# Performance work log

Hardware: AMD Instinct MI355X
Metric: run time of the kernel (lower is better)

The kernel has to match this reference:

```python
import jax, jax.numpy as jnp
import numpy as np

N_NODES = 50000


def gcn_conv(x, W, b, src, dst):
    # PyG GCNConv: h = x @ W; add self-loops; norm = deg^{-1/2}[src]*deg^{-1/2}[dst];
    # out = scatter_add(norm * h[src] -> dst) + bias
    h = x @ W  # [N, out]
    ones = jnp.ones(src.shape[0], dtype=x.dtype)
    deg = jax.ops.segment_sum(ones, dst, num_segments=N_NODES) + 1.0  # +1 for self-loop
    inv_sqrt = deg ** -0.5
    norm = inv_sqrt[src] * inv_sqrt[dst]  # [E]
    msgs = h[src] * norm[:, None]  # [E, out]
    agg = jax.ops.segment_sum(msgs, dst, num_segments=N_NODES)
    # self-loop contribution: norm_ii = deg_i^{-1}
    agg = agg + h * (inv_sqrt * inv_sqrt)[:, None]
    return agg + b


def setup_inputs() -> dict:
    key = jax.random.key(0)
    k1, k2, k3, k4 = jax.random.split(key, 4)
    d_in, d_h = 256, 256
    x = jax.random.normal(k1, (N_NODES, d_in), dtype=jnp.float32)
    edge_index = jax.random.randint(k2, (2, 800000), 0, N_NODES, dtype=jnp.int64)
    # Glorot-style params (GCNConv linear has no bias; separate bias added post-agg)
    W1 = jax.random.normal(k3, (d_in, d_h), dtype=jnp.float32) / np.sqrt(d_in)
    W2 = jax.random.normal(k4, (d_h, d_h), dtype=jnp.float32) / np.sqrt(d_h)
    b1 = jnp.zeros((d_h,), dtype=jnp.float32)
    b2 = jnp.zeros((d_h,), dtype=jnp.float32)
    return {"x": x, "edge_index": edge_index, "W1": W1, "b1": b1, "W2": W2, "b2": b2}


def reference(x, edge_index, W1, b1, W2, b2):
    src, dst = edge_index[0], edge_index[1]
    h = jax.nn.relu(gcn_conv(x, W1, b1, src, dst))
    h = jax.nn.relu(gcn_conv(h, W2, b2, src, dst))
    # global_mean_pool with batch=arange(N) assigns each node its own graph -> identity
    return h
```

## Files before the change

### kernel.cpp

```cpp
#include <hip/hip_runtime.h>
#include <hip/hip_bf16.h>

typedef unsigned short u16;
typedef unsigned int u32;

#define N_NODES 50000
#define N_EDGES 800000
#define DHID 256
#define NCHUNK 49

typedef __attribute__((ext_vector_type(8))) _Float16 f16x8;
typedef __attribute__((ext_vector_type(4))) float f32x4;
typedef __attribute__((ext_vector_type(2))) float f32x2;

__device__ __forceinline__ u16 f2bf(float f) {
    u32 u = __float_as_uint(f);
    u32 r = (u + 0x7FFFu + ((u >> 16) & 1u)) >> 16;
    return (u16)r;
}
__device__ __forceinline__ float bf2f(u32 bits16) {
    return __uint_as_float(bits16 << 16);
}
__device__ __forceinline__ u16 f2h(float f) {
    _Float16 h = (_Float16)f;
    union { _Float16 h; u16 u; } c; c.h = h;
    return c.u;
}
__device__ __forceinline__ void gl_lds16(const void* g, void* l) {
    __builtin_amdgcn_global_load_lds(
        (const __attribute__((address_space(1))) u32*)g,
        (__attribute__((address_space(3))) u32*)l, 16, 0, 0);
}

#define SPLIT_BLKS 12500
#define ZERO_BLKS 196
__global__ void prep_fused(const float* __restrict__ x, u16* __restrict__ xf,
                           const float* __restrict__ W1, const float* __restrict__ W2,
                           u16* __restrict__ W1t, u16* __restrict__ W2t,
                           int* __restrict__ deg, u32* __restrict__ hszero) {
    const int b = blockIdx.x, tid = threadIdx.x;
    if (b < SPLIT_BLKS) {
        int i = b * 256 + tid;
        float4 v = ((const float4*)x)[i];
        u16 h0 = f2h(v.x), h1 = f2h(v.y), h2 = f2h(v.z), h3 = f2h(v.w);
        uint2 hv;
        hv.x = (u32)h0 | ((u32)h1 << 16);
        hv.y = (u32)h2 | ((u32)h3 << 16);
        ((uint2*)xf)[i] = hv;
    } else if (b < SPLIT_BLKS + ZERO_BLKS) {
        int j = (b - SPLIT_BLKS) * 256 + tid;
        if (j < N_NODES) deg[j] = 0;
        if (j < 128) hszero[j] = 0;
    } else {
        int idx = b - (SPLIT_BLKS + ZERO_BLKS);
        int y = idx >> 8, n = idx & 255, k = tid;
        const float* W = y ? W2 : W1;
        u16* o = y ? W2t : W1t;
        o[n * 256 + k] = f2h(W[k * 256 + n]);
    }
}

__global__ void deg_kernel(const int* __restrict__ dst, int* __restrict__ deg, int E) {
    int e = blockIdx.x * 256 + threadIdx.x;
    if (e < E) atomicAdd(&deg[dst[e]], 1);
}

__global__ __launch_bounds__(1024) void scan1_kernel(const int* __restrict__ deg,
                                                     int* __restrict__ partial,
                                                     int* __restrict__ totals, int n) {
    __shared__ int wsum[16];
    __shared__ int woff[16];
    const int tid = threadIdx.x, lane = tid & 63, wid = tid >> 6;
    const int idx = blockIdx.x * 1024 + tid;
    int v = (idx < n) ? deg[idx] : 0;
    int x = v;
#pragma unroll
    for (int off = 1; off < 64; off <<= 1) {
        int t = __shfl_up(x, off, 64);
        if (lane >= off) x += t;
    }
    if (lane == 63) wsum[wid] = x;
    __syncthreads();
    if (tid == 0) {
        int s = 0;
#pragma unroll
        for (int w = 0; w < 16; ++w) { woff[w] = s; s += wsum[w]; }
    }
    __syncthreads();
    x += woff[wid];
    partial[idx] = x;
    if (tid == 1023) totals[blockIdx.x] = x;
}

__global__ void scan3_kernel(const int* __restrict__ deg, const int* __restrict__ partial,
                             const int* __restrict__ totals, int* __restrict__ rptr,
                             int* __restrict__ cursor, int n) {
    __shared__ int coff_s;
    const int tid = threadIdx.x;
    const int mychunk = blockIdx.x >> 2;
    if (tid < 64) {
        int v = (tid < NCHUNK) ? totals[tid] : 0;
        int x = v;
#pragma unroll
        for (int off = 1; off < 64; off <<= 1) {
            int t = __shfl_up(x, off, 64);
            if (tid >= off) x += t;
        }
        if (tid == mychunk) coff_s = x - v;
    }
    __syncthreads();
    int i = blockIdx.x * 256 + tid;
    if (i < n) {
        int e = coff_s + partial[i] - deg[i];
        rptr[i] = e;
        cursor[i] = e;
    }
    if (i == 0) rptr[n] = N_EDGES;
}

__global__ void fill_kernel(const int* __restrict__ src, const int* __restrict__ dst,
                            int* __restrict__ cursor, u16* __restrict__ col16, int E) {
    int e = blockIdx.x * 256 + threadIdx.x;
    if (e < E) {
        int p = atomicAdd(&cursor[dst[e]], 1);
        col16[p] = (u16)src[e];
    }
}

__global__ __launch_bounds__(256) void gemm_f16_kernel(
    const u16* __restrict__ Af, const u16* __restrict__ Bt,
    const int* __restrict__ deg, u16* __restrict__ out, int M) {
    __shared__ u16 As[128 * 32];
    __shared__ u16 Bs[128 * 32];
    const int tid = threadIdx.x;
    const int wave = tid >> 6;
    const int lane = tid & 63;
    const int wm = wave >> 1, wn = wave & 1;
    const int quad = lane >> 4, l16 = lane & 15;
    const int m0 = blockIdx.x * 128;
    const int n0 = blockIdx.y * 128;

    f32x4 acc[4][4] = {};

    const int row0 = tid >> 2, row1 = (256 + tid) >> 2;
    const int kk = (tid & 3) * 8;
    int ar0 = m0 + row0; if (ar0 >= M) ar0 = M - 1;
    int ar1 = m0 + row1; if (ar1 >= M) ar1 = M - 1;
    const size_t aoff0 = (size_t)ar0 * 256 + kk;
    const size_t aoff1 = (size_t)ar1 * 256 + kk;
    const size_t boff0 = (size_t)(n0 + row0) * 256 + kk;
    const size_t boff1 = (size_t)(n0 + row1) * 256 + kk;
    const size_t l0 = (size_t)(wave * 64) * 8;
    const size_t l1 = (size_t)(256 + wave * 64) * 8;

    for (int ko = 0; ko < 8; ++ko) {
        const int koff = ko * 32;
        __syncthreads();
        gl_lds16(Af + aoff0 + koff, &As[l0]);
        gl_lds16(Af + aoff1 + koff, &As[l1]);
        gl_lds16(Bt + boff0 + koff, &Bs[l0]);
        gl_lds16(Bt + boff1 + koff, &Bs[l1]);
        asm volatile("s_waitcnt vmcnt(0)" ::: "memory");
        __syncthreads();

        f16x8 af[4], bf[4];
#pragma unroll
        for (int mi = 0; mi < 4; ++mi)
            af[mi] = *(const f16x8*)&As[(wm * 64 + mi * 16 + l16) * 32 + quad * 8];
#pragma unroll
        for (int ni = 0; ni < 4; ++ni)
            bf[ni] = *(const f16x8*)&Bs[(wn * 64 + ni * 16 + l16) * 32 + quad * 8];
#pragma unroll
        for (int mi = 0; mi < 4; ++mi)
#pragma unroll
            for (int ni = 0; ni < 4; ++ni)
                acc[mi][ni] = __builtin_amdgcn_mfma_f32_16x16x32_f16(af[mi], bf[ni], acc[mi][ni], 0, 0, 0);
    }

#pragma unroll
    for (int mi = 0; mi < 4; ++mi) {
#pragma unroll
        for (int r = 0; r < 4; ++r) {
            int row = m0 + wm * 64 + mi * 16 + quad * 4 + r;
            if (row < M) {
                float s = rsqrtf((float)deg[row] + 1.0f);
#pragma unroll
                for (int ni = 0; ni < 4; ++ni) {
                    int c = n0 + wn * 64 + ni * 16 + l16;
                    out[(size_t)row * 256 + c] = f2bf(acc[mi][ni][r] * s);
                }
            }
        }
    }
}

__global__ __launch_bounds__(256) void agg_kernel(
    const u16* __restrict__ hs, const int* __restrict__ rptr, const u16* __restrict__ col16,
    const int* __restrict__ deg, const float* __restrict__ bias,
    u16* __restrict__ out_f16, float* __restrict__ out_f,
    int mode, int Nn) {
    const int wave = threadIdx.x >> 6, lane = threadIdx.x & 63;
    const int i = blockIdx.x * 4 + wave;
    if (i >= Nn) return;

    const int beg = rptr[i], end = rptr[i + 1];
    const int cnt = end - beg;
    int entry = Nn;
    if (lane == 0) entry = i;
    else if (lane - 1 < cnt) entry = (int)col16[beg + lane - 1];
    int entries = cnt + 1;
    if (entries > 64) entries = 64;
    const int nb = (entries + 3) >> 2;
    const size_t lofs = (size_t)lane * 4;

    f32x2 a01 = {0.f, 0.f}, a23 = {0.f, 0.f};

#define ISSUE(b, x0, x1, x2, x3)                                                \
    {                                                                           \
        int e0 = __builtin_amdgcn_readlane(entry, (b) * 4 + 0);                 \
        int e1 = __builtin_amdgcn_readlane(entry, (b) * 4 + 1);                 \
        int e2 = __builtin_amdgcn_readlane(entry, (b) * 4 + 2);                 \
        int e3 = __builtin_amdgcn_readlane(entry, (b) * 4 + 3);                 \
        x0 = *(const uint2*)(hs + (size_t)e0 * 256 + lofs);                     \
        x1 = *(const uint2*)(hs + (size_t)e1 * 256 + lofs);                     \
        x2 = *(const uint2*)(hs + (size_t)e2 * 256 + lofs);                     \
        x3 = *(const uint2*)(hs + (size_t)e3 * 256 + lofs);                     \
    }
#define ACCUM(v)                                                                \
    {                                                                           \
        f32x2 p0, p1;                                                           \
        p0.x = __uint_as_float(v.x << 16);                                      \
        p0.y = __uint_as_float(v.x & 0xffff0000u);                              \
        p1.x = __uint_as_float(v.y << 16);                                      \
        p1.y = __uint_as_float(v.y & 0xffff0000u);                              \
        a01 += p0; a23 += p1;                                                   \
    }

    uint2 c0, c1, c2, c3, n0v, n1v, n2v, n3v;
    ISSUE(0, c0, c1, c2, c3);
    for (int b = 0; b < nb; ++b) {
        const bool more = (b + 1 < nb);
        if (more) ISSUE(b + 1, n0v, n1v, n2v, n3v);
        ACCUM(c0); ACCUM(c1); ACCUM(c2); ACCUM(c3);
        if (more) { c0 = n0v; c1 = n1v; c2 = n2v; c3 = n3v; }
    }
    for (int j = beg + 63; j < end; ++j) {
        int s = (int)col16[j];
        uint2 v = *(const uint2*)(hs + (size_t)s * 256 + lofs);
        ACCUM(v);
    }
#undef ISSUE
#undef ACCUM

    const float inv = rsqrtf((float)deg[i] + 1.0f);
    float4 bb = *(const float4*)(bias + lane * 4);
    float r0 = fmaxf(fmaf(a01.x, inv, bb.x), 0.0f);
    float r1 = fmaxf(fmaf(a01.y, inv, bb.y), 0.0f);
    float r2 = fmaxf(fmaf(a23.x, inv, bb.z), 0.0f);
    float r3 = fmaxf(fmaf(a23.y, inv, bb.w), 0.0f);
    const size_t o = (size_t)i * 256 + lane * 4;
    if (mode == 0) {
        u16 h0 = f2h(r0), h1 = f2h(r1), h2 = f2h(r2), h3 = f2h(r3);
        uint2 w;
        w.x = (u32)h0 | ((u32)h1 << 16);
        w.y = (u32)h2 | ((u32)h3 << 16);
        *(uint2*)(out_f16 + o) = w;
    } else {
        *(float4*)(out_f + o) = make_float4(r0, r1, r2, r3);
    }
}

extern "C" void kernel_launch(void* const* d_in, const int* in_sizes, int n_in,
                              void* d_out, int out_size, void* d_ws, size_t ws_size,
                              hipStream_t stream) {
    const float* x = (const float*)d_in[0];
    const int* ei = (const int*)d_in[1];
    const float* W1 = (const float*)d_in[2];
    const float* b1 = (const float*)d_in[3];
    const float* W2 = (const float*)d_in[4];
    const float* b2 = (const float*)d_in[5];
    float* out = (float*)d_out;

    const int Nn = N_NODES, E = N_EDGES;
    const int* srcp = ei;
    const int* dstp = ei + E;

    u16* Af = (u16*)d_out;

    char* p = (char*)d_ws;
    auto take = [&](size_t bytes) -> void* {
        void* r = (void*)p;
        p += (bytes + 255) & ~(size_t)255;
        return r;
    };
    u16* hs      = (u16*)take((size_t)(Nn + 1) * DHID * 2);
    u16* col16   = (u16*)take((size_t)E * 2);
    int* deg     = (int*)take((size_t)Nn * 4);
    int* cursor  = (int*)take((size_t)Nn * 4);
    int* rptr    = (int*)take((size_t)(Nn + 1) * 4);
    int* partial = (int*)take((size_t)NCHUNK * 1024 * 4);
    int* totals  = (int*)take(64 * 4);
    u16* W1t     = (u16*)take(256 * 256 * 2);
    u16* W2t     = (u16*)take(256 * 256 * 2);

    prep_fused<<<SPLIT_BLKS + ZERO_BLKS + 512, 256, 0, stream>>>(
        x, Af, W1, W2, W1t, W2t, deg, (u32*)(hs + (size_t)Nn * DHID));
    deg_kernel<<<E / 256, 256, 0, stream>>>(dstp, deg, E);
    scan1_kernel<<<NCHUNK, 1024, 0, stream>>>(deg, partial, totals, Nn);
    scan3_kernel<<<ZERO_BLKS, 256, 0, stream>>>(deg, partial, totals, rptr, cursor, Nn);
    fill_kernel<<<E / 256, 256, 0, stream>>>(srcp, dstp, cursor, col16, E);

    const int gm = (Nn + 127) / 128;
    gemm_f16_kernel<<<dim3(gm, 2), 256, 0, stream>>>(Af, W1t, deg, hs, Nn);
    agg_kernel<<<(Nn + 3) / 4, 256, 0, stream>>>(hs, rptr, col16, deg, b1, Af, nullptr, 0, Nn);
    gemm_f16_kernel<<<dim3(gm, 2), 256, 0, stream>>>(Af, W2t, deg, hs, Nn);
    agg_kernel<<<(Nn + 3) / 4, 256, 0, stream>>>(hs, rptr, col16, deg, b2, nullptr, out, 1, Nn);
}
```

Measured before the change: 342.9 us.

## Store scaled features column-tiled and aggregate per 32-column tile across nodes

The GEMM now writes the normalized hidden features into eight column tiles of 32 features, each laid out contiguously over all nodes plus a zero row. The aggregation kernel assigns each block one tile and 32 nodes, with 8 lanes per node, so the gathered working set per tile is about 3.2 MB and can stay in cache. This replaces one wave per node reading full 512-byte rows. Degree is taken from the row-pointer count instead of reading deg. In exchange, each group of 8 lanes loops to the largest neighbour count among the 8 nodes in its wave, and the edge indices and row pointers are read eight times, once per tile.

```diff
diff --git a/kernel.cpp b/kernel.cpp
--- a/kernel.cpp
+++ b/kernel.cpp
@@ -37,7 +37,7 @@
 __global__ void prep_fused(const float* __restrict__ x, u16* __restrict__ xf,
                            const float* __restrict__ W1, const float* __restrict__ W2,
                            u16* __restrict__ W1t, u16* __restrict__ W2t,
-                           int* __restrict__ deg, u32* __restrict__ hszero) {
+                           int* __restrict__ deg, u32* __restrict__ hs32) {
     const int b = blockIdx.x, tid = threadIdx.x;
     if (b < SPLIT_BLKS) {
         int i = b * 256 + tid;
@@ -50,7 +50,10 @@
     } else if (b < SPLIT_BLKS + ZERO_BLKS) {
         int j = (b - SPLIT_BLKS) * 256 + tid;
         if (j < N_NODES) deg[j] = 0;
-        if (j < 128) hszero[j] = 0;
+        if (j < 128) {
+            int t = j >> 4, w = j & 15;
+            hs32[((size_t)t * (N_NODES + 1) + N_NODES) * 16 + w] = 0;
+        }
     } else {
         int idx = b - (SPLIT_BLKS + ZERO_BLKS);
         int y = idx >> 8, n = idx & 255, k = tid;
@@ -187,7 +190,8 @@
 #pragma unroll
                 for (int ni = 0; ni < 4; ++ni) {
                     int c = n0 + wn * 64 + ni * 16 + l16;
-                    out[(size_t)row * 256 + c] = f2bf(acc[mi][ni][r] * s);
+                    out[((size_t)(c >> 5) * (N_NODES + 1) + row) * 32 + (c & 31)] =
+                        f2bf(acc[mi][ni][r] * s);
                 }
             }
         }
@@ -196,77 +200,83 @@
 
 __global__ __launch_bounds__(256) void agg_kernel(
     const u16* __restrict__ hs, const int* __restrict__ rptr, const u16* __restrict__ col16,
-    const int* __restrict__ deg, const float* __restrict__ bias,
+    const float* __restrict__ bias,
     u16* __restrict__ out_f16, float* __restrict__ out_f,
     int mode, int Nn) {
     const int wave = threadIdx.x >> 6, lane = threadIdx.x & 63;
-    const int i = blockIdx.x * 4 + wave;
-    if (i >= Nn) return;
-
-    const int beg = rptr[i], end = rptr[i + 1];
-    const int cnt = end - beg;
-    int entry = Nn;
-    if (lane == 0) entry = i;
-    else if (lane - 1 < cnt) entry = (int)col16[beg + lane - 1];
-    int entries = cnt + 1;
-    if (entries > 64) entries = 64;
-    const int nb = (entries + 3) >> 2;
-    const size_t lofs = (size_t)lane * 4;
+    const int t = blockIdx.x & 7;
+    const int g = lane >> 3, ql = lane & 7;
+    const int i = (blockIdx.x >> 3) * 32 + wave * 8 + g;
+    const bool valid = (i < Nn);
+    const int ii = valid ? i : (Nn - 1);
+    const int beg = rptr[ii];
+    const int cnt = rptr[ii + 1] - beg;
+    int mc = cnt;
+    mc = max(mc, __shfl_xor(mc, 8, 64));
+    mc = max(mc, __shfl_xor(mc, 16, 64));
+    mc = max(mc, __shfl_xor(mc, 32, 64));
+    const u16* tbase = hs + (size_t)t * (N_NODES + 1) * 32;
+    const int lq = ql * 4;
 
     f32x2 a01 = {0.f, 0.f}, a23 = {0.f, 0.f};
-
-#define ISSUE(b, x0, x1, x2, x3)                                                \
-    {                                                                           \
-        int e0 = __builtin_amdgcn_readlane(entry, (b) * 4 + 0);                 \
-        int e1 = __builtin_amdgcn_readlane(entry, (b) * 4 + 1);                 \
-        int e2 = __builtin_amdgcn_readlane(entry, (b) * 4 + 2);                 \
-        int e3 = __builtin_amdgcn_readlane(entry, (b) * 4 + 3);                 \
-        x0 = *(const uint2*)(hs + (size_t)e0 * 256 + lofs);                     \
-        x1 = *(const uint2*)(hs + (size_t)e1 * 256 + lofs);                     \
-        x2 = *(const uint2*)(hs + (size_t)e2 * 256 + lofs);                     \
-        x3 = *(const uint2*)(hs + (size_t)e3 * 256 + lofs);                     \
-    }
-#define ACCUM(v)                                                                \
-    {                                                                           \
-        f32x2 p0, p1;                                                           \
-        p0.x = __uint_as_float(v.x << 16);                                      \
-        p0.y = __uint_as_float(v.x & 0xffff0000u);                              \
-        p1.x = __uint_as_float(v.y << 16);                                      \
-        p1.y = __uint_as_float(v.y & 0xffff0000u);                              \
-        a01 += p0; a23 += p1;                                                   \
-    }
-
-    uint2 c0, c1, c2, c3, n0v, n1v, n2v, n3v;
-    ISSUE(0, c0, c1, c2, c3);
-    for (int b = 0; b < nb; ++b) {
-        const bool more = (b + 1 < nb);
-        if (more) ISSUE(b + 1, n0v, n1v, n2v, n3v);
-        ACCUM(c0); ACCUM(c1); ACCUM(c2); ACCUM(c3);
-        if (more) { c0 = n0v; c1 = n1v; c2 = n2v; c3 = n3v; }
-    }
-    for (int j = beg + 63; j < end; ++j) {
-        int s = (int)col16[j];
-        uint2 v = *(const uint2*)(hs + (size_t)s * 256 + lofs);
-        ACCUM(v);
-    }
-#undef ISSUE
+    const uint2 vself = *(const uint2*)(tbase + (size_t)ii * 32 + lq);
+
+#define GIDX(j, e)                                                      \
+    {                                                                   \
+        int p = min((j), cnt - 1); p = max(p, 0);                       \
+        int id = (int)col16[beg + p];                                   \
+        e = ((j) < cnt) ? id : Nn;                                      \
+    }
+#define LOADP(e) (*(const uint2*)(tbase + (size_t)(e) * 32 + lq))
+#define ACCUM(v)                                                        \
+    {                                                                   \
+        f32x2 p0, p1;                                                   \
+        p0.x = __uint_as_float(v.x << 16);                              \
+        p0.y = __uint_as_float(v.x & 0xffff0000u);                      \
+        p1.x = __uint_as_float(v.y << 16);                              \
+        p1.y = __uint_as_float(v.y & 0xffff0000u);                      \
+        a01 += p0; a23 += p1;                                           \
+    }
+
+    if (mc > 0) {
+        int e1;
+        uint2 vA;
+        { int e0; GIDX(0, e0); vA = LOADP(e0); }
+        GIDX(1, e1);
+        for (int j = 0; j < mc; ++j) {
+            uint2 vB = {0, 0};
+            int e2 = Nn;
+            if (j + 1 < mc) {
+                vB = LOADP(e1);
+                GIDX(j + 2, e2);
+            }
+            ACCUM(vA);
+            vA = vB; e1 = e2;
+        }
+    }
+    ACCUM(vself);
+#undef GIDX
+#undef LOADP
 #undef ACCUM
 
-    const float inv = rsqrtf((float)deg[i] + 1.0f);
-    float4 bb = *(const float4*)(bias + lane * 4);
+    const float inv = rsqrtf((float)cnt + 1.0f);
+    const float4 bb = *(const float4*)(bias + t * 32 + lq);
     float r0 = fmaxf(fmaf(a01.x, inv, bb.x), 0.0f);
     float r1 = fmaxf(fmaf(a01.y, inv, bb.y), 0.0f);
     float r2 = fmaxf(fmaf(a23.x, inv, bb.z), 0.0f);
     float r3 = fmaxf(fmaf(a23.y, inv, bb.w), 0.0f);
-    const size_t o = (size_t)i * 256 + lane * 4;
-    if (mode == 0) {
-        u16 h0 = f2h(r0), h1 = f2h(r1), h2 = f2h(r2), h3 = f2h(r3);
-        uint2 w;
-        w.x = (u32)h0 | ((u32)h1 << 16);
-        w.y = (u32)h2 | ((u32)h3 << 16);
-        *(uint2*)(out_f16 + o) = w;
-    } else {
-        *(float4*)(out_f + o) = make_float4(r0, r1, r2, r3);
+
+    if (valid) {
+        const size_t o = (size_t)i * 256 + t * 32 + lq;
+        if (mode == 0) {
+            u16 h0 = f2h(r0), h1 = f2h(r1), h2 = f2h(r2), h3 = f2h(r3);
+            uint2 w;
+            w.x = (u32)h0 | ((u32)h1 << 16);
+            w.y = (u32)h2 | ((u32)h3 << 16);
+            *(uint2*)(out_f16 + o) = w;
+        } else {
+            *(float4*)(out_f + o) = make_float4(r0, r1, r2, r3);
+        }
     }
 }
 
@@ -293,7 +303,7 @@
         p += (bytes + 255) & ~(size_t)255;
         return r;
     };
-    u16* hs      = (u16*)take((size_t)(Nn + 1) * DHID * 2);
+    u16* hs      = (u16*)take((size_t)8 * (Nn + 1) * 32 * 2);
     u16* col16   = (u16*)take((size_t)E * 2);
     int* deg     = (int*)take((size_t)Nn * 4);
     int* cursor  = (int*)take((size_t)Nn * 4);
@@ -304,15 +314,16 @@
     u16* W2t     = (u16*)take(256 * 256 * 2);
 
     prep_fused<<<SPLIT_BLKS + ZERO_BLKS + 512, 256, 0, stream>>>(
-        x, Af, W1, W2, W1t, W2t, deg, (u32*)(hs + (size_t)Nn * DHID));
+        x, Af, W1, W2, W1t, W2t, deg, (u32*)hs);
     deg_kernel<<<E / 256, 256, 0, stream>>>(dstp, deg, E);
     scan1_kernel<<<NCHUNK, 1024, 0, stream>>>(deg, partial, totals, Nn);
     scan3_kernel<<<ZERO_BLKS, 256, 0, stream>>>(deg, partial, totals, rptr, cursor, Nn);
     fill_kernel<<<E / 256, 256, 0, stream>>>(srcp, dstp, cursor, col16, E);
 
     const int gm = (Nn + 127) / 128;
+    const int aggblocks = ((Nn + 31) / 32) * 8;
     gemm_f16_kernel<<<dim3(gm, 2), 256, 0, stream>>>(Af, W1t, deg, hs, Nn);
-    agg_kernel<<<(Nn + 3) / 4, 256, 0, stream>>>(hs, rptr, col16, deg, b1, Af, nullptr, 0, Nn);
+    agg_kernel<<<aggblocks, 256, 0, stream>>>(hs, rptr, col16, b1, Af, nullptr, 0, Nn);
     gemm_f16_kernel<<<dim3(gm, 2), 256, 0, stream>>>(Af, W2t, deg, hs, Nn);
-    agg_kernel<<<(Nn + 3) / 4, 256, 0, stream>>>(hs, rptr, col16, deg, b2, nullptr, out, 1, Nn);
-}
+    agg_kernel<<<aggblocks, 256, 0, stream>>>(hs, rptr, col16, b2, nullptr, out, 1, Nn);
+}
```

Result: slower. 359.7 us (+4.9%).
